# Kernel tuning notes

Hardware: AMD Instinct MI355X
Metric: run time of the kernel (lower is better)

## Reference

```python
import jax, jax.numpy as jnp
import numpy as np

B, N, E, H = 4, 1024, 512, 8
D = E // H  # head_dim = 64


def setup_inputs() -> dict:
    key = jax.random.key(0)
    ks = jax.random.split(key, 8)
    s = 1.0 / np.sqrt(E)
    return {
        "X": jax.random.normal(ks[0], (B, N, E), jnp.float32),
        "real_nodes": jnp.ones((B, N), jnp.float32),
        "attn_add": jax.random.normal(ks[1], (B, H, N, N), jnp.float32),
        "attn_mult": jax.random.uniform(ks[2], (B, H, N, N), jnp.float32),
        "Wq": jax.random.normal(ks[3], (E, E), jnp.float32) * s,
        "bq": jnp.zeros((E,), jnp.float32),
        "Wk": jax.random.normal(ks[4], (E, E), jnp.float32) * s,
        "bk": jnp.zeros((E,), jnp.float32),
        "Wv": jax.random.normal(ks[5], (E, E), jnp.float32) * s,
        "bv": jnp.zeros((E,), jnp.float32),
        "Wo": jax.random.normal(ks[6], (E, E), jnp.float32) * s,
        "bo": jnp.zeros((E,), jnp.float32),
    }


def reference(X, real_nodes, attn_add, attn_mult, Wq, bq, Wk, bk, Wv, bv, Wo, bo):
    b, n, e = X.shape
    # torch nn.Linear: y = x @ W.T + b ; split heads -> [B,H,N,D]
    q = (X @ Wq.T + bq).reshape(b, n, H, D).transpose(0, 2, 1, 3)
    k = (X @ Wk.T + bk).reshape(b, n, H, D).transpose(0, 2, 1, 3)
    v = (X @ Wv.T + bv).reshape(b, n, H, D).transpose(0, 2, 1, 3)
    score = jnp.einsum("bhqd,bhkd->bhqk", q, k) / jnp.sqrt(jnp.float32(D))
    # real_nodes -> [B,1,N,1]: scales whole query rows of the score matrix
    score = score * real_nodes[:, None, :, None]
    score = score + attn_add
    attn = jax.nn.softmax(score, axis=-1)
    attn = attn * attn_mult  # post-softmax multiplicative mask
    out = jnp.einsum("bhqk,bhkd->bhqd", attn, v)
    out = out.transpose(0, 2, 1, 3).reshape(b, n, e)
    return out @ Wo.T + bo
```

## Files before the change

kernel.cpp:

```cpp
#include <hip/hip_runtime.h>

#define B_ 4
#define N_ 1024
#define E_ 512
#define H_ 8
#define D_ 64
#define BH_ 32
#define KVB 32

typedef __bf16 bf16;
typedef __bf16 bf16x8 __attribute__((ext_vector_type(8)));
typedef __bf16 bf16x4 __attribute__((ext_vector_type(4)));
typedef float f32x4 __attribute__((ext_vector_type(4)));

#define MFMA16 __builtin_amdgcn_mfma_f32_16x16x32_bf16

typedef const __attribute__((address_space(1))) void* gas_t;
typedef __attribute__((address_space(3))) void* las_t;

__device__ __forceinline__ void gload16(const void* g, void* l) {
    __builtin_amdgcn_global_load_lds((gas_t)g, (las_t)l, 16, 0, 0);
}

__global__ __launch_bounds__(256) void prep_all(
    const float* __restrict__ X, const float* __restrict__ Wq,
    const float* __restrict__ Wk, const float* __restrict__ Wv,
    const float* __restrict__ Wo,
    bf16* __restrict__ Xh, bf16* __restrict__ Xl,
    bf16* __restrict__ Wqh, bf16* __restrict__ Wql,
    bf16* __restrict__ Wkh, bf16* __restrict__ Wkl,
    bf16* __restrict__ Wvh,
    bf16* __restrict__ Woh, bf16* __restrict__ Wol)
{
    const int NX = B_ * N_ * E_;
    const int NW = E_ * E_;
    int i = blockIdx.x * 256 + threadIdx.x;
    if (i < NX) {
        float x = X[i]; bf16 h = (bf16)x;
        Xh[i] = h; Xl[i] = (bf16)(x - (float)h);
        return;
    }
    i -= NX;
    int w = i >> 18, j = i & (NW - 1);
    if (w == 0) { float x = Wq[j]; bf16 h = (bf16)x; Wqh[j] = h; Wql[j] = (bf16)(x - (float)h); }
    else if (w == 1) { float x = Wk[j]; bf16 h = (bf16)x; Wkh[j] = h; Wkl[j] = (bf16)(x - (float)h); }
    else if (w == 2) { float x = Wv[j]; Wvh[j] = (bf16)x; }
    else if (w == 3) { float x = Wo[j]; bf16 h = (bf16)x; Woh[j] = h; Wol[j] = (bf16)(x - (float)h); }
}

__global__ __launch_bounds__(256) void qkv_gemm(
    const bf16* __restrict__ Xh, const bf16* __restrict__ Xl,
    const bf16* __restrict__ Wqh, const bf16* __restrict__ Wql, const float* __restrict__ bq,
    const bf16* __restrict__ Wkh, const bf16* __restrict__ Wkl, const float* __restrict__ bk,
    const bf16* __restrict__ Wvh, const float* __restrict__ bvv,
    bf16* __restrict__ Qh, bf16* __restrict__ Ql,
    bf16* __restrict__ Kh, bf16* __restrict__ Kl,
    bf16* __restrict__ Vt)
{
    __shared__ alignas(16) bf16 wlds[2][2][64 * 32];
    __shared__ alignas(16) bf16 tlds[64 * 72];
    const int z = blockIdx.z;
    const int e0 = blockIdx.x * 64;
    const int m0 = blockIdx.y * 64;
    const int tid = threadIdx.x;
    const int w = tid >> 6, l = tid & 63, lr = l & 15, lg = l >> 4;
    const int h = e0 >> 6;
    const bool three = (z != 2);

    const bf16* Wh = (z == 0) ? Wqh : ((z == 1) ? Wkh : Wvh);
    const bf16* Wl = (z == 0) ? Wql : ((z == 1) ? Wkl : Wqh );

    const int wrow = 16 * w + (l >> 2);
    const int wcol = 8 * ((l & 3) ^ ((l >> 3) & 3));
    const bf16* whsrc = Wh + (size_t)(e0 + wrow) * E_ + wcol;
    const bf16* wlsrc = Wl + (size_t)(e0 + wrow) * E_ + wcol;

#define WSTAGE(k0, bi) do {                                  \
        gload16(whsrc + (k0), &wlds[bi][0][w * 512]);        \
        if (three) gload16(wlsrc + (k0), &wlds[bi][1][w * 512]); \
    } while (0)

    WSTAGE(0, 0);

    f32x4 acc[4] = {};
    const bf16* xh = &Xh[(size_t)(m0 + w * 16 + lr) * E_];
    const bf16* xl = &Xl[(size_t)(m0 + w * 16 + lr) * E_];

    for (int it = 0; it < 16; ++it) {
        const int k0 = it * 32;
        const int bi = it & 1;
        if (it < 15) {
            WSTAGE(k0 + 32, bi ^ 1);
            __builtin_amdgcn_sched_barrier(0);
            if (three) asm volatile("s_waitcnt vmcnt(2)" ::: "memory");
            else       asm volatile("s_waitcnt vmcnt(1)" ::: "memory");
        } else {
            asm volatile("s_waitcnt vmcnt(0)" ::: "memory");
        }
        __builtin_amdgcn_sched_barrier(0);
        __builtin_amdgcn_s_barrier();

        bf16x8 ah = *(const bf16x8*)(xh + k0 + lg * 8);
        bf16x8 al = three ? *(const bf16x8*)(xl + k0 + lg * 8) : ah;

        const char* whb = (const char*)&wlds[bi][0][0];
        const char* wlb = (const char*)&wlds[bi][1][0];
        const int wsw = ((lr >> 1) & 3) << 4;
#pragma unroll
        for (int t = 0; t < 4; ++t) {
            int rb = (16 * t + lr) * 64;
            bf16x8 bh = *(const bf16x8*)(whb + rb + ((lg * 16) ^ wsw));
            acc[t] = MFMA16(ah, bh, acc[t], 0, 0, 0);
            if (three) {
                bf16x8 bl = *(const bf16x8*)(wlb + rb + ((lg * 16) ^ wsw));
                acc[t] = MFMA16(al, bh, acc[t], 0, 0, 0);
                acc[t] = MFMA16(ah, bl, acc[t], 0, 0, 0);
            }
        }
        __builtin_amdgcn_s_barrier();
    }
#undef WSTAGE

    if (z == 2) {
        const float* bias = bvv;
#pragma unroll
        for (int t = 0; t < 4; ++t) {
            float bv = bias[e0 + 16 * t + lr];
#pragma unroll
            for (int r = 0; r < 4; ++r)
                tlds[(16 * t + lr) * 72 + w * 16 + lg * 4 + r] = (bf16)(acc[t][r] + bv);
        }
        __syncthreads();
        int d = tid >> 2, c0 = (tid & 3) * 16;
        int b = m0 >> 10, n = (m0 & (N_ - 1)) + c0;
        bf16x8* dst = (bf16x8*)&Vt[((size_t)(b * H_ + h) * D_ + d) * N_ + n];
        const bf16x8* s = (const bf16x8*)&tlds[d * 72 + c0];
        dst[0] = s[0];
        dst[1] = s[1];
        return;
    }

    const float* bias = z ? bk : bq;
    bf16* Oh = z ? Kh : Qh;
    bf16* Ol = z ? Kl : Ql;
#pragma unroll
    for (int t = 0; t < 4; ++t) {
        float bv = bias[e0 + 16 * t + lr];
#pragma unroll
        for (int r = 0; r < 4; ++r) {
            int m = m0 + w * 16 + lg * 4 + r;
            int b = m >> 10, n = m & (N_ - 1);
            float v = acc[t][r] + bv;
            bf16 hi = (bf16)v;
            size_t idx = ((size_t)(b * H_ + h) * N_ + n) * D_ + 16 * t + lr;
            Oh[idx] = hi;
            Ol[idx] = (bf16)(v - (float)hi);
        }
    }
}

__global__ __launch_bounds__(256) void attn_kernel(
    const bf16* __restrict__ Qh_, const bf16* __restrict__ Ql_,
    const bf16* __restrict__ Kh_, const bf16* __restrict__ Kl_,
    const bf16* __restrict__ Vt_,
    const float* __restrict__ rn,
    const float* __restrict__ addm, const float* __restrict__ multm,
    float* __restrict__ Opart, float* __restrict__ Mb, float* __restrict__ Lb,
    int ch)
{
    __shared__ alignas(16) float mlds[4][2][2][16 * 32];
    __shared__ alignas(16) bf16 khlds[2][32 * 64];
    __shared__ alignas(16) bf16 kllds[2][32 * 64];
    __shared__ alignas(16) bf16 plds[4][16 * 40];

    const int by = blockIdx.y;
    const int bh = by & (BH_ - 1), c = by >> 5;
    const int b = bh >> 3;
    const int kvb = c * ch;
    const int tid = threadIdx.x;
    const int w = tid >> 6, l = tid & 63, lr = l & 15, lg = l >> 4;
    const int q0 = blockIdx.x * 64 + w * 16;
    bf16* pw = &plds[w][0];

    const bf16* qb = &Qh_[((size_t)bh * N_ + q0 + lr) * D_];
    const bf16* qlb = &Ql_[((size_t)bh * N_ + q0 + lr) * D_];
    bf16x8 qh0 = *(const bf16x8*)(qb + lg * 8);
    bf16x8 qh1 = *(const bf16x8*)(qb + 32 + lg * 8);
    bf16x8 ql0 = *(const bf16x8*)(qlb + lg * 8);
    bf16x8 ql1 = *(const bf16x8*)(qlb + 32 + lg * 8);

    const float rnq = rn[b * N_ + q0 + lr] * 0.125f;

    float mrun = -3e38f, lrun = 0.f;
    f32x4 acc[4] = {};

    const size_t mb0 = (size_t)bh * N_ * N_;
    const int mrow = l >> 3, mcol = 4 * ((l & 7) ^ ((l >> 3) & 7));
    const float* asrc = addm + mb0 + (size_t)(q0 + mrow) * N_ + mcol;
    const float* msrc = multm + mb0 + (size_t)(q0 + mrow) * N_ + mcol;
    const int krow = 8 * w + (l >> 3), kcol = 8 * ((l & 7) ^ ((l >> 3) & 7));
    const bf16* khsrc = Kh_ + ((size_t)bh * N_ + krow) * D_ + kcol;
    const bf16* klsrc = Kl_ + ((size_t)bh * N_ + krow) * D_ + kcol;
    const bf16* vbase = Vt_ + ((size_t)bh * D_ + lr) * N_ + 8 * lg;

#define STAGE(kv, bi)                                                     \
    do {                                                                  \
        gload16(asrc + (kv), &mlds[w][bi][0][0]);                         \
        gload16(asrc + (kv) + 8 * N_, &mlds[w][bi][0][256]);              \
        gload16(msrc + (kv), &mlds[w][bi][1][0]);                         \
        gload16(msrc + (kv) + 8 * N_, &mlds[w][bi][1][256]);              \
        gload16(khsrc + (size_t)(kv) * D_, &khlds[bi][w * 512]);          \
        gload16(klsrc + (size_t)(kv) * D_, &kllds[bi][w * 512]);          \
    } while (0)

    STAGE(kvb, 0);

    const int nt = ch / KVB;
    for (int tile = 0; tile < nt; ++tile) {
        const int kv0 = kvb + tile * KVB;
        const int bi = tile & 1;

        if (tile + 1 < nt) {
            STAGE(kv0 + KVB, bi ^ 1);
            __builtin_amdgcn_sched_barrier(0);
            asm volatile("s_waitcnt vmcnt(6)" ::: "memory");
        } else {
            asm volatile("s_waitcnt vmcnt(0)" ::: "memory");
        }
        __builtin_amdgcn_sched_barrier(0);
        __builtin_amdgcn_s_barrier();

        bf16x8 vv[4];
#pragma unroll
        for (int t = 0; t < 4; ++t)
            vv[t] = *(const bf16x8*)(vbase + (size_t)(16 * t) * N_ + kv0);
        __builtin_amdgcn_sched_barrier(0);

        const char* khb = (const char*)&khlds[bi][0];
        const char* klb = (const char*)&kllds[bi][0];
        const int ksw = (lr & 7) << 4;
        bf16x8 kh[2][2], kl[2][2];
#pragma unroll
        for (int t = 0; t < 2; ++t) {
            int rb = (16 * t + lr) * 128;
            kh[t][0] = *(const bf16x8*)(khb + rb + ((lg * 16) ^ ksw));
            kh[t][1] = *(const bf16x8*)(khb + rb + ((64 + lg * 16) ^ ksw));
            kl[t][0] = *(const bf16x8*)(klb + rb + ((lg * 16) ^ ksw));
            kl[t][1] = *(const bf16x8*)(klb + rb + ((64 + lg * 16) ^ ksw));
        }

        f32x4 z[2];
#pragma unroll
        for (int t = 0; t < 2; ++t) {
            f32x4 zz = {};
            zz = MFMA16(kh[t][0], qh0, zz, 0, 0, 0);
            zz = MFMA16(kh[t][1], qh1, zz, 0, 0, 0);
            zz = MFMA16(kh[t][0], ql0, zz, 0, 0, 0);
            zz = MFMA16(kh[t][1], ql1, zz, 0, 0, 0);
            zz = MFMA16(kl[t][0], qh0, zz, 0, 0, 0);
            zz = MFMA16(kl[t][1], qh1, zz, 0, 0, 0);
            z[t] = zz;
        }

        const float* at = &mlds[w][bi][0][0];
        const float* mt = &mlds[w][bi][1][0];
        f32x4 ma[2], mm[2];
#pragma unroll
        for (int t = 0; t < 2; ++t) {
            int woff = lr * 32 + ((16 * t + 4 * lg) ^ ((lr & 7) << 2));
            ma[t] = *(const f32x4*)(at + woff);
            mm[t] = *(const f32x4*)(mt + woff);
        }

        float sv[2][4];
#pragma unroll
        for (int t = 0; t < 2; ++t)
#pragma unroll
            for (int r = 0; r < 4; ++r)
                sv[t][r] = z[t][r] * rnq + ma[t][r];

        float vmax = sv[0][0];
#pragma unroll
        for (int t = 0; t < 2; ++t)
#pragma unroll
            for (int r = 0; r < 4; ++r) vmax = fmaxf(vmax, sv[t][r]);
        vmax = fmaxf(vmax, __shfl_xor(vmax, 16));
        vmax = fmaxf(vmax, __shfl_xor(vmax, 32));
        float mn = fmaxf(mrun, vmax);
        float rs = __expf(mrun - mn);
        mrun = mn;
        lrun *= rs;
#pragma unroll
        for (int t = 0; t < 4; ++t) acc[t] *= rs;
        float pe[2][4];
        float rsum = 0.f;
#pragma unroll
        for (int t = 0; t < 2; ++t)
#pragma unroll
            for (int r = 0; r < 4; ++r) { pe[t][r] = __expf(sv[t][r] - mn); rsum += pe[t][r]; }
        rsum += __shfl_xor(rsum, 16);
        rsum += __shfl_xor(rsum, 32);
        lrun += rsum;

#pragma unroll
        for (int t = 0; t < 2; ++t) {
            bf16x4 pk;
#pragma unroll
            for (int r = 0; r < 4; ++r) pk[r] = (bf16)(pe[t][r] * mm[t][r]);
            *(bf16x4*)(pw + lr * 40 + 16 * t + 4 * lg) = pk;
        }

        bf16x8 pa = *(const bf16x8*)(pw + lr * 40 + 8 * lg);
#pragma unroll
        for (int t = 0; t < 4; ++t)
            acc[t] = MFMA16(vv[t], pa, acc[t], 0, 0, 0);

        __builtin_amdgcn_s_barrier();
    }

    const size_t cb = ((size_t)c * BH_ + bh) * N_;
    float* ob = &Opart[(cb + q0 + lr) * D_];
#pragma unroll
    for (int t = 0; t < 4; ++t)
        *(f32x4*)(ob + 16 * t + 4 * lg) = acc[t];
    if (lg == 0) {
        Mb[cb + q0 + lr] = mrun;
        Lb[cb + q0 + lr] = lrun;
    }
#undef STAGE
}

__global__ __launch_bounds__(256) void merge_kernel(
    const float* __restrict__ Opart, const float* __restrict__ Mb,
    const float* __restrict__ Lb,
    bf16* __restrict__ AOh, bf16* __restrict__ AOl, int ks)
{
    int idx = blockIdx.x * 256 + threadIdx.x;
    int bh = idx >> 14;
    int rem = idx & 16383;
    int q = rem >> 4, d4 = rem & 15;

    float M = -3e38f;
    for (int c = 0; c < ks; ++c)
        M = fmaxf(M, Mb[((size_t)c * BH_ + bh) * N_ + q]);
    float L = 0.f;
    f32x4 o = {};
    for (int c = 0; c < ks; ++c) {
        size_t base = ((size_t)c * BH_ + bh) * N_ + q;
        float wgt = __expf(Mb[base] - M);
        L += wgt * Lb[base];
        f32x4 v = *(const f32x4*)&Opart[base * D_ + d4 * 4];
        o += wgt * v;
    }
    float inv = 1.f / L;
    int b = bh >> 3, h = bh & 7;
    size_t ob = ((size_t)b * N_ + q) * E_ + h * D_ + d4 * 4;
    bf16x4 hi, lo;
#pragma unroll
    for (int j = 0; j < 4; ++j) {
        float x = o[j] * inv;
        bf16 hh = (bf16)x;
        hi[j] = hh;
        lo[j] = (bf16)(x - (float)hh);
    }
    *(bf16x4*)&AOh[ob] = hi;
    *(bf16x4*)&AOl[ob] = lo;
}

__global__ __launch_bounds__(256) void out_gemm(
    const bf16* __restrict__ Ah, const bf16* __restrict__ Al,
    const bf16* __restrict__ Wh, const bf16* __restrict__ Wl,
    const float* __restrict__ bias,
    float* __restrict__ out)
{
    __shared__ alignas(16) bf16 wlds[2][2][64 * 32];
    const int e0 = blockIdx.x * 64;
    const int m0 = blockIdx.y * 64;
    const int tid = threadIdx.x;
    const int w = tid >> 6, l = tid & 63, lr = l & 15, lg = l >> 4;

    const int wrow = 16 * w + (l >> 2);
    const int wcol = 8 * ((l & 3) ^ ((l >> 3) & 3));
    const bf16* whsrc = Wh + (size_t)(e0 + wrow) * E_ + wcol;
    const bf16* wlsrc = Wl + (size_t)(e0 + wrow) * E_ + wcol;

#define WSTAGE(k0, bi) do {                               \
        gload16(whsrc + (k0), &wlds[bi][0][w * 512]);     \
        gload16(wlsrc + (k0), &wlds[bi][1][w * 512]);     \
    } while (0)

    WSTAGE(0, 0);

    f32x4 acc[4] = {};
    const bf16* ah_p = &Ah[(size_t)(m0 + w * 16 + lr) * E_];
    const bf16* al_p = &Al[(size_t)(m0 + w * 16 + lr) * E_];

    for (int it = 0; it < 16; ++it) {
        const int k0 = it * 32;
        const int bi = it & 1;
        if (it < 15) {
            WSTAGE(k0 + 32, bi ^ 1);
            __builtin_amdgcn_sched_barrier(0);
            asm volatile("s_waitcnt vmcnt(2)" ::: "memory");
        } else {
            asm volatile("s_waitcnt vmcnt(0)" ::: "memory");
        }
        __builtin_amdgcn_sched_barrier(0);
        __builtin_amdgcn_s_barrier();

        bf16x8 ah = *(const bf16x8*)(ah_p + k0 + lg * 8);
        bf16x8 al = *(const bf16x8*)(al_p + k0 + lg * 8);
        const char* whb = (const char*)&wlds[bi][0][0];
        const char* wlb = (const char*)&wlds[bi][1][0];
        const int wsw = ((lr >> 1) & 3) << 4;
#pragma unroll
        for (int t = 0; t < 4; ++t) {
            int rb = (16 * t + lr) * 64;
            bf16x8 bh = *(const bf16x8*)(whb + rb + ((lg * 16) ^ wsw));
            bf16x8 bl = *(const bf16x8*)(wlb + rb + ((lg * 16) ^ wsw));
            acc[t] = MFMA16(ah, bh, acc[t], 0, 0, 0);
            acc[t] = MFMA16(al, bh, acc[t], 0, 0, 0);
            acc[t] = MFMA16(ah, bl, acc[t], 0, 0, 0);
        }
        __builtin_amdgcn_s_barrier();
    }
#undef WSTAGE

#pragma unroll
    for (int t = 0; t < 4; ++t) {
        float bv = bias[e0 + 16 * t + lr];
#pragma unroll
        for (int r = 0; r < 4; ++r) {
            int m = m0 + w * 16 + lg * 4 + r;
            out[(size_t)m * E_ + e0 + 16 * t + lr] = acc[t][r] + bv;
        }
    }
}

extern "C" void kernel_launch(void* const* d_in, const int* in_sizes, int n_in,
                              void* d_out, int out_size, void* d_ws, size_t ws_size,
                              hipStream_t stream) {
    const float* X = (const float*)d_in[0];
    const float* rn = (const float*)d_in[1];
    const float* addm = (const float*)d_in[2];
    const float* multm = (const float*)d_in[3];
    const float* Wq = (const float*)d_in[4];
    const float* bq = (const float*)d_in[5];
    const float* Wk = (const float*)d_in[6];
    const float* bk = (const float*)d_in[7];
    const float* Wv = (const float*)d_in[8];
    const float* bv = (const float*)d_in[9];
    const float* Wo = (const float*)d_in[10];
    const float* bo = (const float*)d_in[11];
    float* out = (float*)d_out;

    const size_t SZ_X = (size_t)B_ * N_ * E_;
    const size_t SZ_W = (size_t)E_ * E_;

    bf16* p = (bf16*)d_ws;
    bf16* Xh = p;  p += SZ_X;
    bf16* Xl = p;  p += SZ_X;
    bf16* Wqh = p; p += SZ_W;
    bf16* Wql = p; p += SZ_W;
    bf16* Wkh = p; p += SZ_W;
    bf16* Wkl = p; p += SZ_W;
    bf16* Wvh = p; p += SZ_W;
    bf16* Woh = p; p += SZ_W;
    bf16* Wol = p; p += SZ_W;
    bf16* Qh = p;  p += SZ_X;
    bf16* Ql = p;  p += SZ_X;
    bf16* Kh = p;  p += SZ_X;
    bf16* Kl = p;  p += SZ_X;
    bf16* Vt = p;  p += SZ_X;
    bf16* AOh = p; p += SZ_X;
    bf16* AOl = p; p += SZ_X;

    size_t fixed_bytes = (size_t)((char*)p - (char*)d_ws);
    size_t per_ks = (size_t)BH_ * N_ * D_ * 4 + (size_t)BH_ * N_ * 2 * 4;
    int ks = 4;
    if (fixed_bytes + 4 * per_ks > ws_size) ks = 2;
    if (fixed_bytes + 2 * per_ks > ws_size) ks = 1;

    float* Opart = (float*)p;
    float* Mb = Opart + (size_t)ks * BH_ * N_ * D_;
    float* Lb = Mb + (size_t)ks * BH_ * N_;

    const int NPREP = B_ * N_ * E_ + 4 * E_ * E_;
    prep_all<<<dim3(NPREP / 256), 256, 0, stream>>>(X, Wq, Wk, Wv, Wo,
        Xh, Xl, Wqh, Wql, Wkh, Wkl, Wvh, Woh, Wol);

    dim3 gq(E_ / 64, (B_ * N_) / 64, 3);
    qkv_gemm<<<gq, 256, 0, stream>>>(Xh, Xl, Wqh, Wql, bq, Wkh, Wkl, bk, Wvh, bv,
                                     Qh, Ql, Kh, Kl, Vt);

    attn_kernel<<<dim3(N_ / 64, ks * BH_), 256, 0, stream>>>(
        Qh, Ql, Kh, Kl, Vt, rn, addm, multm, Opart, Mb, Lb, N_ / ks);

    merge_kernel<<<dim3((BH_ * N_ * (D_ / 4)) / 256), 256, 0, stream>>>(
        Opart, Mb, Lb, AOh, AOl, ks);

    dim3 gg(E_ / 64, (B_ * N_) / 64);
    out_gemm<<<gg, 256, 0, stream>>>(AOh, AOl, Woh, Wol, bo, out);
}
```

Before: 157.4 us.

## Split attention KV across waves per 16-query block, stage masks in wide rows

The attention kernel now gives each block 16 query rows, with its four waves each covering a different 32-key slice of a 128-key step, in place of four waves each holding separate query rows. K and V are read straight from global memory into registers rather than staged through LDS. Only the add/mult masks, now full 128-wide rows, are double-buffered in LDS. Each wave writes its own partial softmax state, so the merge kernel combines four times as many chunks (ks*4) and the KV split count drops to 2. The aim is more contiguous mask streaming and more blocks in flight (launch bounds ask for 3 per CU), at the cost of more partial-output traffic and a heavier merge.

```diff
diff --git a/kernel.cpp b/kernel.cpp
--- a/kernel.cpp
+++ b/kernel.cpp
@@ -6,7 +6,6 @@
 #define H_ 8
 #define D_ 64
 #define BH_ 32
-#define KVB 32
 
 typedef __bf16 bf16;
 typedef __bf16 bf16x8 __attribute__((ext_vector_type(8)));
@@ -159,7 +158,7 @@
     }
 }
 
-__global__ __launch_bounds__(256) void attn_kernel(
+__global__ __launch_bounds__(256, 3) void attn_kernel(
     const bf16* __restrict__ Qh_, const bf16* __restrict__ Ql_,
     const bf16* __restrict__ Kh_, const bf16* __restrict__ Kl_,
     const bf16* __restrict__ Vt_,
@@ -168,9 +167,8 @@
     float* __restrict__ Opart, float* __restrict__ Mb, float* __restrict__ Lb,
     int ch)
 {
-    __shared__ alignas(16) float mlds[4][2][2][16 * 32];
-    __shared__ alignas(16) bf16 khlds[2][32 * 64];
-    __shared__ alignas(16) bf16 kllds[2][32 * 64];
+    __shared__ alignas(16) float alds[2][16 * 128];
+    __shared__ alignas(16) float mlds[2][16 * 128];
     __shared__ alignas(16) bf16 plds[4][16 * 40];
 
     const int by = blockIdx.y;
@@ -179,7 +177,7 @@
     const int kvb = c * ch;
     const int tid = threadIdx.x;
     const int w = tid >> 6, l = tid & 63, lr = l & 15, lg = l >> 4;
-    const int q0 = blockIdx.x * 64 + w * 16;
+    const int q0 = blockIdx.x * 16;
     bf16* pw = &plds[w][0];
 
     const bf16* qb = &Qh_[((size_t)bh * N_ + q0 + lr) * D_];
@@ -195,59 +193,58 @@
     f32x4 acc[4] = {};
 
     const size_t mb0 = (size_t)bh * N_ * N_;
-    const int mrow = l >> 3, mcol = 4 * ((l & 7) ^ ((l >> 3) & 7));
-    const float* asrc = addm + mb0 + (size_t)(q0 + mrow) * N_ + mcol;
-    const float* msrc = multm + mb0 + (size_t)(q0 + mrow) * N_ + mcol;
-    const int krow = 8 * w + (l >> 3), kcol = 8 * ((l & 7) ^ ((l >> 3) & 7));
-    const bf16* khsrc = Kh_ + ((size_t)bh * N_ + krow) * D_ + kcol;
-    const bf16* klsrc = Kl_ + ((size_t)bh * N_ + krow) * D_ + kcol;
-    const bf16* vbase = Vt_ + ((size_t)bh * D_ + lr) * N_ + 8 * lg;
-
-#define STAGE(kv, bi)                                                     \
-    do {                                                                  \
-        gload16(asrc + (kv), &mlds[w][bi][0][0]);                         \
-        gload16(asrc + (kv) + 8 * N_, &mlds[w][bi][0][256]);              \
-        gload16(msrc + (kv), &mlds[w][bi][1][0]);                         \
-        gload16(msrc + (kv) + 8 * N_, &mlds[w][bi][1][256]);              \
-        gload16(khsrc + (size_t)(kv) * D_, &khlds[bi][w * 512]);          \
-        gload16(klsrc + (size_t)(kv) * D_, &kllds[bi][w * 512]);          \
-    } while (0)
-
-    STAGE(kvb, 0);
-
-    const int nt = ch / KVB;
-    for (int tile = 0; tile < nt; ++tile) {
-        const int kv0 = kvb + tile * KVB;
-        const int bi = tile & 1;
-
-        if (tile + 1 < nt) {
-            STAGE(kv0 + KVB, bi ^ 1);
+    const int r1 = l >> 5;
+    const int cbyte = (l & 31) * 16;
+    const float* aRow = addm + mb0 + (size_t)(q0 + r1) * N_;
+    const float* mRow = multm + mb0 + (size_t)(q0 + r1) * N_;
+
+#define MSTAGE(kv, bi_)                                                        \
+    {                                                                          \
+        _Pragma("unroll")                                                      \
+        for (int j = 0; j < 2; ++j) {                                          \
+            const int i = 2 * w + j;                                           \
+            const int sw = cbyte ^ ((((i << 1) + r1) & 7) << 4);               \
+            gload16((const char*)(aRow + (size_t)(2 * i) * N_ + (kv)) + sw,    \
+                    &alds[bi_][i * 256]);                                      \
+            gload16((const char*)(mRow + (size_t)(2 * i) * N_ + (kv)) + sw,    \
+                    &mlds[bi_][i * 256]);                                      \
+        }                                                                      \
+    }
+
+    MSTAGE(kvb, 0);
+
+    const int nt = ch / 128;
+    for (int s = 0; s < nt; ++s) {
+        const int kv0 = kvb + s * 128;
+        const int bi = s & 1;
+        const bool more = (s + 1 < nt);
+        const int kw = kv0 + 32 * w;
+
+        const bf16* kbase = Kh_ + ((size_t)bh * N_ + kw + lr) * D_ + 8 * lg;
+        const bf16* klbase = Kl_ + ((size_t)bh * N_ + kw + lr) * D_ + 8 * lg;
+        bf16x8 kh[2][2], kl[2][2];
+#pragma unroll
+        for (int t = 0; t < 2; ++t) {
+            kh[t][0] = *(const bf16x8*)(kbase + (size_t)(16 * t) * D_);
+            kh[t][1] = *(const bf16x8*)(kbase + (size_t)(16 * t) * D_ + 32);
+            kl[t][0] = *(const bf16x8*)(klbase + (size_t)(16 * t) * D_);
+            kl[t][1] = *(const bf16x8*)(klbase + (size_t)(16 * t) * D_ + 32);
+        }
+        bf16x8 vv[4];
+#pragma unroll
+        for (int t = 0; t < 4; ++t)
+            vv[t] = *(const bf16x8*)(Vt_ + ((size_t)bh * D_ + 16 * t + lr) * N_ + kw + 8 * lg);
+        __builtin_amdgcn_sched_barrier(0);
+
+        if (more) {
+            MSTAGE(kv0 + 128, bi ^ 1);
             __builtin_amdgcn_sched_barrier(0);
-            asm volatile("s_waitcnt vmcnt(6)" ::: "memory");
+            asm volatile("s_waitcnt vmcnt(16)" ::: "memory");
         } else {
-            asm volatile("s_waitcnt vmcnt(0)" ::: "memory");
+            asm volatile("s_waitcnt vmcnt(12)" ::: "memory");
         }
         __builtin_amdgcn_sched_barrier(0);
         __builtin_amdgcn_s_barrier();
-
-        bf16x8 vv[4];
-#pragma unroll
-        for (int t = 0; t < 4; ++t)
-            vv[t] = *(const bf16x8*)(vbase + (size_t)(16 * t) * N_ + kv0);
-        __builtin_amdgcn_sched_barrier(0);
-
-        const char* khb = (const char*)&khlds[bi][0];
-        const char* klb = (const char*)&kllds[bi][0];
-        const int ksw = (lr & 7) << 4;
-        bf16x8 kh[2][2], kl[2][2];
-#pragma unroll
-        for (int t = 0; t < 2; ++t) {
-            int rb = (16 * t + lr) * 128;
-            kh[t][0] = *(const bf16x8*)(khb + rb + ((lg * 16) ^ ksw));
-            kh[t][1] = *(const bf16x8*)(khb + rb + ((64 + lg * 16) ^ ksw));
-            kl[t][0] = *(const bf16x8*)(klb + rb + ((lg * 16) ^ ksw));
-            kl[t][1] = *(const bf16x8*)(klb + rb + ((64 + lg * 16) ^ ksw));
-        }
 
         f32x4 z[2];
 #pragma unroll
@@ -262,14 +259,14 @@
             z[t] = zz;
         }
 
-        const float* at = &mlds[w][bi][0][0];
-        const float* mt = &mlds[w][bi][1][0];
+        const char* ab = (const char*)&alds[bi][0];
+        const char* mb_ = (const char*)&mlds[bi][0];
         f32x4 ma[2], mm[2];
 #pragma unroll
         for (int t = 0; t < 2; ++t) {
-            int woff = lr * 32 + ((16 * t + 4 * lg) ^ ((lr & 7) << 2));
-            ma[t] = *(const f32x4*)(at + woff);
-            mm[t] = *(const f32x4*)(mt + woff);
+            int off = lr * 512 + ((((32 * w + 16 * t + 4 * lg) * 4)) ^ ((lr & 7) << 4));
+            ma[t] = *(const f32x4*)(ab + off);
+            mm[t] = *(const f32x4*)(mb_ + off);
         }
 
         float sv[2][4];
@@ -318,16 +315,16 @@
         __builtin_amdgcn_s_barrier();
     }
 
-    const size_t cb = ((size_t)c * BH_ + bh) * N_;
-    float* ob = &Opart[(cb + q0 + lr) * D_];
+    const size_t cb2 = ((size_t)(c * 4 + w) * BH_ + bh) * N_;
+    float* ob = &Opart[(cb2 + q0 + lr) * D_];
 #pragma unroll
     for (int t = 0; t < 4; ++t)
         *(f32x4*)(ob + 16 * t + 4 * lg) = acc[t];
     if (lg == 0) {
-        Mb[cb + q0 + lr] = mrun;
-        Lb[cb + q0 + lr] = lrun;
-    }
-#undef STAGE
+        Mb[cb2 + q0 + lr] = mrun;
+        Lb[cb2 + q0 + lr] = lrun;
+    }
+#undef MSTAGE
 }
 
 __global__ __launch_bounds__(256) void merge_kernel(
@@ -476,14 +473,14 @@
     bf16* AOl = p; p += SZ_X;
 
     size_t fixed_bytes = (size_t)((char*)p - (char*)d_ws);
-    size_t per_ks = (size_t)BH_ * N_ * D_ * 4 + (size_t)BH_ * N_ * 2 * 4;
-    int ks = 4;
-    if (fixed_bytes + 4 * per_ks > ws_size) ks = 2;
-    if (fixed_bytes + 2 * per_ks > ws_size) ks = 1;
+    size_t per_chunk = (size_t)BH_ * N_ * D_ * 4 + (size_t)BH_ * N_ * 2 * 4;
+    int ks = 2;
+    if (fixed_bytes + (size_t)(ks * 4) * per_chunk > ws_size) ks = 1;
+    const int nchunk = ks * 4;
 
     float* Opart = (float*)p;
-    float* Mb = Opart + (size_t)ks * BH_ * N_ * D_;
-    float* Lb = Mb + (size_t)ks * BH_ * N_;
+    float* Mb = Opart + (size_t)nchunk * BH_ * N_ * D_;
+    float* Lb = Mb + (size_t)nchunk * BH_ * N_;
 
     const int NPREP = B_ * N_ * E_ + 4 * E_ * E_;
     prep_all<<<dim3(NPREP / 256), 256, 0, stream>>>(X, Wq, Wk, Wv, Wo,
@@ -493,11 +490,11 @@
     qkv_gemm<<<gq, 256, 0, stream>>>(Xh, Xl, Wqh, Wql, bq, Wkh, Wkl, bk, Wvh, bv,
                                      Qh, Ql, Kh, Kl, Vt);
 
-    attn_kernel<<<dim3(N_ / 64, ks * BH_), 256, 0, stream>>>(
+    attn_kernel<<<dim3(N_ / 16, BH_ * ks), 256, 0, stream>>>(
         Qh, Ql, Kh, Kl, Vt, rn, addm, multm, Opart, Mb, Lb, N_ / ks);
 
     merge_kernel<<<dim3((BH_ * N_ * (D_ / 4)) / 256), 256, 0, stream>>>(
-        Opart, Mb, Lb, AOh, AOl, ks);
+        Opart, Mb, Lb, AOh, AOl, nchunk);
 
     dim3 gg(E_ / 64, (B_ * N_) / 64);
     out_gemm<<<gg, 256, 0, stream>>>(AOh, AOl, Woh, Wol, bo, out);
```

Result: slower. 199.9 us (+27.0%).
